# Optimization experiments

Hardware: AMD Instinct MI355X
Metric: run time of the kernel (lower is better)

## Reference

```python
import itertools
import jax, jax.numpy as jnp
import numpy as np

B, S, D = 512, 49, 448
H, KD, RATIO, RES = 8, 32, 4, 7
EKD = KD * RATIO              # expanded key dim = 128
QKV_OUT = H * (2 * KD + EKD)  # 1536
MLP_HID = D * 4               # 1792
EPS = 1e-5
LS_INIT = 1e-5


def _build_bias_idxs():
    points = list(itertools.product(range(RES), range(RES)))
    offsets = {}
    idxs = []
    for p1 in points:
        for p2 in points:
            off = (abs(p1[0] - p2[0]), abs(p1[1] - p2[1]))
            if off not in offsets:
                offsets[off] = len(offsets)
            idxs.append(offsets[off])
    return np.asarray(idxs, dtype=np.int32).reshape(len(points), len(points)), len(offsets)


def setup_inputs() -> dict:
    key = jax.random.key(0)
    ks = jax.random.split(key, 10)
    idxs_np, n_off = _build_bias_idxs()  # (49,49), 49 unique offsets
    std = 0.02
    return {
        "hidden_states": jax.random.normal(ks[0], (B, S, D), jnp.float32),
        "ln1_g": jnp.ones((D,), jnp.float32),
        "ln1_b": jnp.zeros((D,), jnp.float32),
        "qkv_w": jax.random.normal(ks[1], (D, QKV_OUT), jnp.float32) * std,
        "qkv_b": jnp.zeros((QKV_OUT,), jnp.float32),
        "attention_biases": jax.random.normal(ks[2], (H, n_off), jnp.float32) * std,
        "proj_w": jax.random.normal(ks[3], (H * EKD, D), jnp.float32) * std,
        "proj_b": jnp.zeros((D,), jnp.float32),
        "ln2_g": jnp.ones((D,), jnp.float32),
        "ln2_b": jnp.zeros((D,), jnp.float32),
        "mlp_w1": jax.random.normal(ks[4], (D, MLP_HID), jnp.float32) * std,
        "mlp_b1": jnp.zeros((MLP_HID,), jnp.float32),
        "mlp_w2": jax.random.normal(ks[5], (MLP_HID, D), jnp.float32) * std,
        "mlp_b2": jnp.zeros((D,), jnp.float32),
        "ls1": jnp.full((D,), LS_INIT, jnp.float32),
        "ls2": jnp.full((D,), LS_INIT, jnp.float32),
        "attention_bias_idxs": jnp.asarray(idxs_np),
    }


def _layernorm(x, g, b):
    mu = jnp.mean(x, axis=-1, keepdims=True)
    var = jnp.mean(jnp.square(x - mu), axis=-1, keepdims=True)
    return (x - mu) * jax.lax.rsqrt(var + EPS) * g + b


def reference(hidden_states, ln1_g, ln1_b, qkv_w, qkv_b, attention_biases,
              proj_w, proj_b, ln2_g, ln2_b, mlp_w1, mlp_b1, mlp_w2, mlp_b2,
              ls1, ls2, attention_bias_idxs):
    x = hidden_states
    # --- token mixer (self-attention with relative-position bias) ---
    h = _layernorm(x, ln1_g, ln1_b)
    qkv = h @ qkv_w + qkv_b                           # [B,S,1536]
    qkv = qkv.reshape(B, S, H, 2 * KD + EKD)
    q, k, v = jnp.split(qkv, [KD, 2 * KD], axis=3)    # [B,S,H,32/32/128]
    scale = KD ** (-0.5)
    scores = jnp.einsum("bqhd,bkhd->bhqk", q, k) * scale
    bias = attention_biases[:, attention_bias_idxs]   # [H,S,S]
    probs = jax.nn.softmax(scores + bias[None], axis=-1)
    ctx = jnp.einsum("bhqk,bkhd->bqhd", probs, v).reshape(B, S, H * EKD)
    attn_out = ctx @ proj_w + proj_b                  # [B,S,D]
    # --- residual with layerscale (drop_path = identity in eval) ---
    x = x + ls1 * attn_out
    # --- MLP branch ---
    h2 = _layernorm(x, ln2_g, ln2_b)
    m = jax.nn.gelu(h2 @ mlp_w1 + mlp_b1, approximate=False)
    m = m @ mlp_w2 + mlp_b2
    x = x + ls2 * m
    return x
```

## Files before the change

kernel.cpp:

```cpp
#include <hip/hip_runtime.h>
#include <hip/hip_bf16.h>

#define BB 512
#define SS 49
#define DD 448
#define HH 8
#define QKVO 1536
#define MLPH 1792
#define MM (BB*SS)

using bf16_t = __hip_bfloat16;
typedef __attribute__((ext_vector_type(8))) short short8;
typedef __attribute__((ext_vector_type(4))) float f32x4;

__device__ __forceinline__ void gload_lds16(const void* g, void* l) {
  __builtin_amdgcn_global_load_lds(
      (const __attribute__((address_space(1))) void*)g,
      (__attribute__((address_space(3))) void*)l,
      16, 0, 0);
}

__global__ void prep_kernel(const float* __restrict__ qkv_w, const float* __restrict__ proj_w,
                            const float* __restrict__ w1, const float* __restrict__ w2,
                            const float* __restrict__ ab, const int* __restrict__ idxs,
                            bf16_t* __restrict__ qkv_wT, bf16_t* __restrict__ proj_wT,
                            bf16_t* __restrict__ w1T, bf16_t* __restrict__ w2T,
                            bf16_t* __restrict__ bias_pad)
{
  int idx = blockIdx.x * 256 + threadIdx.x;
  if (idx < 688128) {
    int n = idx / 448, k = idx % 448;
    qkv_wT[idx] = __float2bfloat16(qkv_w[k*1536 + n]);
  } else if ((idx -= 688128) < 458752) {
    int n = idx / 1024, k = idx % 1024;
    proj_wT[idx] = __float2bfloat16(proj_w[k*448 + n]);
  } else if ((idx -= 458752) < 802816) {
    int n = idx / 448, k = idx % 448;
    w1T[idx] = __float2bfloat16(w1[k*1792 + n]);
  } else if ((idx -= 802816) < 802816) {
    int n = idx / 1792, k = idx % 1792;
    w2T[idx] = __float2bfloat16(w2[k*448 + n]);
  } else if ((idx -= 802816) < 32768) {
    int h = idx >> 12, r = (idx >> 6) & 63, c = idx & 63;
    float v = (r < SS && c < SS) ? ab[h*49 + idxs[r*49 + c]] : -1e30f;
    bias_pad[idx] = __float2bfloat16(v);
  }
}

__global__ __launch_bounds__(256) void ln_kernel(const float* __restrict__ x,
                                                 const float* __restrict__ g,
                                                 const float* __restrict__ b,
                                                 bf16_t* __restrict__ out)
{
  const int w = threadIdx.x >> 6, lane = threadIdx.x & 63;
  const int row = blockIdx.x * 4 + w;
  const float* xr = x + (size_t)row * DD;
  float v[7];
  float s = 0.f;
#pragma unroll
  for (int j = 0; j < 7; ++j) { v[j] = xr[lane + 64*j]; s += v[j]; }
#pragma unroll
  for (int off = 32; off; off >>= 1) s += __shfl_xor(s, off, 64);
  const float mu = s * (1.0f/448.0f);
  float q = 0.f;
#pragma unroll
  for (int j = 0; j < 7; ++j) { float d = v[j] - mu; q += d*d; }
#pragma unroll
  for (int off = 32; off; off >>= 1) q += __shfl_xor(q, off, 64);
  const float rstd = rsqrtf(q * (1.0f/448.0f) + 1e-5f);
  bf16_t* orow = out + (size_t)row * DD;
#pragma unroll
  for (int j = 0; j < 7; ++j) {
    int c = lane + 64*j;
    orow[c] = __float2bfloat16((v[j] - mu) * rstd * g[c] + b[c]);
  }
}

__global__ __launch_bounds__(256) void red1_ln2_kernel(
    const float* __restrict__ x, const bf16_t* __restrict__ p0,
    const bf16_t* __restrict__ p1, const float* __restrict__ pb,
    const float* __restrict__ ls1, const float* __restrict__ g,
    const float* __restrict__ b, float* __restrict__ out, bf16_t* __restrict__ h2)
{
  const int w = threadIdx.x >> 6, lane = threadIdx.x & 63;
  const int row = blockIdx.x * 4 + w;
  const float* xr = x + (size_t)row * DD;
  const bf16_t* p0r = p0 + (size_t)row * DD;
  const bf16_t* p1r = p1 + (size_t)row * DD;
  float* orow = out + (size_t)row * DD;
  float v[7];
  float s = 0.f;
#pragma unroll
  for (int j = 0; j < 7; ++j) {
    const int c = lane + 64*j;
    const float pv = __bfloat162float(p0r[c]) + __bfloat162float(p1r[c]) + pb[c];
    v[j] = xr[c] + ls1[c] * pv;
    orow[c] = v[j];
    s += v[j];
  }
#pragma unroll
  for (int off = 32; off; off >>= 1) s += __shfl_xor(s, off, 64);
  const float mu = s * (1.0f/448.0f);
  float q = 0.f;
#pragma unroll
  for (int j = 0; j < 7; ++j) { float d = v[j] - mu; q += d*d; }
#pragma unroll
  for (int off = 32; off; off >>= 1) q += __shfl_xor(q, off, 64);
  const float rstd = rsqrtf(q * (1.0f/448.0f) + 1e-5f);
  bf16_t* hrow = h2 + (size_t)row * DD;
#pragma unroll
  for (int j = 0; j < 7; ++j) {
    const int c = lane + 64*j;
    hrow[c] = __float2bfloat16((v[j] - mu) * rstd * g[c] + b[c]);
  }
}

__global__ __launch_bounds__(256) void red2_kernel(
    const bf16_t* __restrict__ q0, const bf16_t* __restrict__ q1,
    const float* __restrict__ pb, const float* __restrict__ ls2,
    float* __restrict__ out)
{
  const int w = threadIdx.x >> 6, lane = threadIdx.x & 63;
  const int row = blockIdx.x * 4 + w;
  const bf16_t* q0r = q0 + (size_t)row * DD;
  const bf16_t* q1r = q1 + (size_t)row * DD;
  float* orow = out + (size_t)row * DD;
#pragma unroll
  for (int j = 0; j < 7; ++j) {
    const int c = lane + 64*j;
    const float pv = __bfloat162float(q0r[c]) + __bfloat162float(q1r[c]) + pb[c];
    orow[c] = orow[c] + ls2[c] * pv;
  }
}

enum { EP_BF16 = 0, EP_GELU = 2, EP_PART = 4 };

template<int EPI, int NSPLIT>
__global__ __launch_bounds__(256, 2) void gemmr_bf16(
    const bf16_t* __restrict__ A, const bf16_t* __restrict__ Bt,
    const float* __restrict__ bias, bf16_t* __restrict__ O0,
    bf16_t* __restrict__ O1, int N, int K, int gy)
{
  __shared__ __align__(16) char lds[32768];
  const int t = threadIdx.x;
  const int lane = t & 63;
  const int w = t >> 6;

  const int chunk = gridDim.x >> 3;
  const int swz = (blockIdx.x & 7) * chunk + (blockIdx.x >> 3);
  const int m0 = (swz / (gy * NSPLIT)) * 128;
  const int rr = swz % (gy * NSPLIT);
  const int n0 = (rr / NSPLIT) * 128;
  const int sp = rr % NSPLIT;
  const int ksub = K / NSPLIT;
  const int kbase = sp * ksub;

  const int fr = lane & 15;
  const int fq = lane >> 4;
  const int wm = (w >> 1) * 64;
  const int wn = (w & 1) * 64;

  f32x4 acc[4][4];
#pragma unroll
  for (int i = 0; i < 4; ++i)
#pragma unroll
    for (int j = 0; j < 4; ++j)
      acc[i][j] = f32x4{0.f, 0.f, 0.f, 0.f};

  const int rsub = t >> 3;
  const int g8 = (t & 7) ^ (rsub & 7);
  const int wbase = w * 1024;
  const int nkt = ksub >> 6;

  const bf16_t* gA[4];
  const bf16_t* gB[4];
#pragma unroll
  for (int i = 0; i < 4; ++i) {
    gA[i] = A + (size_t)(m0 + i*32 + rsub) * K + kbase + g8*8;
    int rb = n0 + i*32 + rsub;
    if (rb >= N) rb = N - 1;
    gB[i] = Bt + (size_t)rb * K + kbase + g8*8;
  }

  for (int kt = 0; kt < nkt; ++kt) {
    const int ko = kt << 6;
#pragma unroll
    for (int i = 0; i < 4; ++i) {
      gload_lds16(gA[i] + ko, lds + i*4096 + wbase);
      gload_lds16(gB[i] + ko, lds + 16384 + i*4096 + wbase);
    }
    __syncthreads();
#pragma unroll
    for (int kk = 0; kk < 2; ++kk) {
      short8 af[4], bfr[4];
#pragma unroll
      for (int i = 0; i < 4; ++i) {
        const int ra = wm + i*16 + fr;
        const int ca = (fq + kk*4) ^ (ra & 7);
        af[i] = *(const short8*)(lds + ra*128 + ca*16);
        const int rb2 = wn + i*16 + fr;
        const int cb = (fq + kk*4) ^ (rb2 & 7);
        bfr[i] = *(const short8*)(lds + 16384 + rb2*128 + cb*16);
      }
#pragma unroll
      for (int mi = 0; mi < 4; ++mi)
#pragma unroll
        for (int ni = 0; ni < 4; ++ni)
          acc[mi][ni] = __builtin_amdgcn_mfma_f32_16x16x32_bf16(af[mi], bfr[ni], acc[mi][ni], 0, 0, 0);
    }
    __syncthreads();
  }

  bf16_t* P = (NSPLIT == 2 && sp == 1) ? O1 : O0;
#pragma unroll
  for (int mi = 0; mi < 4; ++mi) {
#pragma unroll
    for (int ni = 0; ni < 4; ++ni) {
      const int col = n0 + wn + ni*16 + fr;
      if (col < N) {
        float bc = 0.f;
        if constexpr (EPI != EP_PART) bc = bias[col];
        const int row0 = m0 + wm + mi*16 + fq*4;
#pragma unroll
        for (int ri = 0; ri < 4; ++ri) {
          const size_t o = (size_t)(row0 + ri) * N + col;
          const float v = acc[mi][ni][ri] + bc;
          if constexpr (EPI == EP_GELU) {
            P[o] = __float2bfloat16(0.5f * v * (1.0f + erff(v * 0.7071067811865475f)));
          } else {
            P[o] = __float2bfloat16(v);
          }
        }
      }
    }
  }
}

__global__ __launch_bounds__(64) void attn_mfma_kernel(const bf16_t* __restrict__ qkv,
                                                       const bf16_t* __restrict__ bias_pad,
                                                       bf16_t* __restrict__ ctx)
{
  __shared__ __align__(16) bf16_t VsF[64*128];
  __shared__ __align__(16) bf16_t PsF[64*72];
  const int b = blockIdx.x >> 3, h = blockIdx.x & 7;
  const int l = threadIdx.x;
  const int fr = l & 15, g = l >> 4;
  const size_t base = ((size_t)b * SS) * QKVO + (size_t)h * 192;

  for (int c = l; c < 1024; c += 64) {
    const int j = c >> 4, ch = c & 15;
    const int jc = j < SS ? j : SS - 1;
    short8 v = *(const short8*)(qkv + base + (size_t)jc * QKVO + 64 + ch*8);
    *(short8*)(&VsF[j*128 + ((ch ^ (j >> 3)) & 15)*8]) = v;
  }

  short8 qf[4], kf[4];
#pragma unroll
  for (int mi = 0; mi < 4; ++mi) {
    int qr = mi*16 + fr; if (qr > SS-1) qr = SS-1;
    qf[mi] = *(const short8*)(qkv + base + (size_t)qr * QKVO + g*8);
    int kr = mi*16 + fr; if (kr > SS-1) kr = SS-1;
    kf[mi] = *(const short8*)(qkv + base + (size_t)kr * QKVO + 32 + g*8);
  }
  f32x4 sc[4][4];
#pragma unroll
  for (int mi = 0; mi < 4; ++mi)
#pragma unroll
    for (int ni = 0; ni < 4; ++ni)
      sc[mi][ni] = f32x4{0.f,0.f,0.f,0.f};
#pragma unroll
  for (int mi = 0; mi < 4; ++mi)
#pragma unroll
    for (int ni = 0; ni < 4; ++ni)
      sc[mi][ni] = __builtin_amdgcn_mfma_f32_16x16x32_bf16(qf[mi], kf[ni], sc[mi][ni], 0, 0, 0);

  const float scale = 0.17677669529663687f;
  const bf16_t* bp = bias_pad + (size_t)h * 4096;
#pragma unroll
  for (int mi = 0; mi < 4; ++mi) {
#pragma unroll
    for (int ri = 0; ri < 4; ++ri) {
      const int r = mi*16 + g*4 + ri;
      float v0 = sc[mi][0][ri]*scale + __bfloat162float(bp[r*64 +      fr]);
      float v1 = sc[mi][1][ri]*scale + __bfloat162float(bp[r*64 + 16 + fr]);
      float v2 = sc[mi][2][ri]*scale + __bfloat162float(bp[r*64 + 32 + fr]);
      float v3 = sc[mi][3][ri]*scale + __bfloat162float(bp[r*64 + 48 + fr]);
      float m = fmaxf(fmaxf(v0, v1), fmaxf(v2, v3));
#pragma unroll
      for (int off = 8; off; off >>= 1) m = fmaxf(m, __shfl_xor(m, off, 64));
      v0 = __expf(v0 - m); v1 = __expf(v1 - m);
      v2 = __expf(v2 - m); v3 = __expf(v3 - m);
      float s = v0 + v1 + v2 + v3;
#pragma unroll
      for (int off = 8; off; off >>= 1) s += __shfl_xor(s, off, 64);
      const float inv = 1.0f / s;
      PsF[r*72 +      fr] = __float2bfloat16(v0 * inv);
      PsF[r*72 + 16 + fr] = __float2bfloat16(v1 * inv);
      PsF[r*72 + 32 + fr] = __float2bfloat16(v2 * inv);
      PsF[r*72 + 48 + fr] = __float2bfloat16(v3 * inv);
    }
  }
  __syncthreads();

  short8 pf[4][2];
#pragma unroll
  for (int mi = 0; mi < 4; ++mi)
#pragma unroll
    for (int ks = 0; ks < 2; ++ks)
      pf[mi][ks] = *(const short8*)(&PsF[(mi*16 + fr)*72 + ks*32 + g*8]);

#pragma unroll
  for (int ni = 0; ni < 8; ++ni) {
    const int e = ni*16 + fr;
    short8 vf[2];
#pragma unroll
    for (int ks = 0; ks < 2; ++ks) {
      const int jb = ks*32 + g*8;
#pragma unroll
      for (int jj = 0; jj < 8; ++jj) {
        const int j = jb + jj;
        const int ch = ((e >> 3) ^ (j >> 3)) & 15;
        vf[ks][jj] = *(const short*)(&VsF[j*128 + ch*8 + (e & 7)]);
      }
    }
    f32x4 acc2[4];
#pragma unroll
    for (int mi = 0; mi < 4; ++mi) acc2[mi] = f32x4{0.f,0.f,0.f,0.f};
#pragma unroll
    for (int ks = 0; ks < 2; ++ks)
#pragma unroll
      for (int mi = 0; mi < 4; ++mi)
        acc2[mi] = __builtin_amdgcn_mfma_f32_16x16x32_bf16(pf[mi][ks], vf[ks], acc2[mi], 0, 0, 0);
#pragma unroll
    for (int mi = 0; mi < 4; ++mi) {
#pragma unroll
      for (int ri = 0; ri < 4; ++ri) {
        const int q = mi*16 + g*4 + ri;
        if (q < SS)
          ctx[((size_t)b * SS + q) * 1024 + h*128 + e] = __float2bfloat16(acc2[mi][ri]);
      }
    }
  }
}

extern "C" void kernel_launch(void* const* d_in, const int* in_sizes, int n_in,
                              void* d_out, int out_size, void* d_ws, size_t ws_size,
                              hipStream_t stream) {
  const float* x      = (const float*)d_in[0];
  const float* ln1_g  = (const float*)d_in[1];
  const float* ln1_b  = (const float*)d_in[2];
  const float* qkv_w  = (const float*)d_in[3];
  const float* qkv_b  = (const float*)d_in[4];
  const float* ab     = (const float*)d_in[5];
  const float* proj_w = (const float*)d_in[6];
  const float* proj_b = (const float*)d_in[7];
  const float* ln2_g  = (const float*)d_in[8];
  const float* ln2_b  = (const float*)d_in[9];
  const float* w1     = (const float*)d_in[10];
  const float* b1     = (const float*)d_in[11];
  const float* w2     = (const float*)d_in[12];
  const float* b2     = (const float*)d_in[13];
  const float* ls1    = (const float*)d_in[14];
  const float* ls2    = (const float*)d_in[15];
  const int*   idxs   = (const int*)d_in[16];
  float* out = (float*)d_out;
  char* ws = (char*)d_ws;

  bf16_t* h_buf    = (bf16_t*)(ws);
  bf16_t* qkv_buf  = (bf16_t*)(ws + 22478848);
  bf16_t* ctx_buf  = (bf16_t*)(ws + 99549184);
  bf16_t* m_buf    = (bf16_t*)(ws + 22478848);
  bf16_t* p0       = (bf16_t*)(ws + 22478848);
  bf16_t* p1       = (bf16_t*)(ws + 44957696);
  bf16_t* q0       = (bf16_t*)(ws);
  bf16_t* q1       = (bf16_t*)(ws + 112394240);
  bf16_t* qkv_wT   = (bf16_t*)(ws + 150929408);
  bf16_t* proj_wT  = (bf16_t*)(ws + 152305664);
  bf16_t* w1T      = (bf16_t*)(ws + 153223168);
  bf16_t* w2T      = (bf16_t*)(ws + 154828800);
  bf16_t* bias_pad = (bf16_t*)(ws + 156434432);

  const int prep_total = 688128 + 458752 + 802816 + 802816 + 32768;
  prep_kernel<<<(prep_total + 255)/256, 256, 0, stream>>>(
      qkv_w, proj_w, w1, w2, ab, idxs, qkv_wT, proj_wT, w1T, w2T, bias_pad);

  ln_kernel<<<MM/4, 256, 0, stream>>>(x, ln1_g, ln1_b, h_buf);

  gemmr_bf16<EP_BF16, 1><<<196*12, 256, 0, stream>>>(
      h_buf, qkv_wT, qkv_b, qkv_buf, nullptr, QKVO, DD, 12);

  attn_mfma_kernel<<<BB*HH, 64, 0, stream>>>(qkv_buf, bias_pad, ctx_buf);

  gemmr_bf16<EP_PART, 2><<<196*4*2, 256, 0, stream>>>(
      ctx_buf, proj_wT, nullptr, p0, p1, DD, 1024, 4);

  red1_ln2_kernel<<<MM/4, 256, 0, stream>>>(
      x, p0, p1, proj_b, ls1, ln2_g, ln2_b, out, h_buf);

  gemmr_bf16<EP_GELU, 1><<<196*14, 256, 0, stream>>>(
      h_buf, w1T, b1, m_buf, nullptr, MLPH, DD, 14);

  gemmr_bf16<EP_PART, 2><<<196*4*2, 256, 0, stream>>>(
      m_buf, w2T, nullptr, q0, q1, DD, MLPH, 4);

  red2_kernel<<<MM/4, 256, 0, stream>>>(q0, q1, b2, ls2, out);
}
```

Baseline: 324.8 us.

## Fuse weight prep with LN1, vectorize residual kernels, use tanh GELU

```diff
diff --git a/kernel.cpp b/kernel.cpp
--- a/kernel.cpp
+++ b/kernel.cpp
@@ -20,40 +20,46 @@
       16, 0, 0);
 }
 
-__global__ void prep_kernel(const float* __restrict__ qkv_w, const float* __restrict__ proj_w,
-                            const float* __restrict__ w1, const float* __restrict__ w2,
-                            const float* __restrict__ ab, const int* __restrict__ idxs,
-                            bf16_t* __restrict__ qkv_wT, bf16_t* __restrict__ proj_wT,
-                            bf16_t* __restrict__ w1T, bf16_t* __restrict__ w2T,
-                            bf16_t* __restrict__ bias_pad)
+__device__ __forceinline__ float fast_gelu(float v) {
+  const float u = 0.7978845608028654f * (v + 0.044715f * v * v * v);
+  const float e = __expf(2.0f * u);
+  return 0.5f * v * (2.0f - 2.0f / (e + 1.0f));
+}
+
+#define PREP_BLOCKS 10880
+__global__ __launch_bounds__(256) void prep_ln1_kernel(
+    const float* __restrict__ qkv_w, const float* __restrict__ proj_w,
+    const float* __restrict__ w1, const float* __restrict__ w2,
+    const float* __restrict__ ab, const int* __restrict__ idxs,
+    bf16_t* __restrict__ qkv_wT, bf16_t* __restrict__ proj_wT,
+    bf16_t* __restrict__ w1T, bf16_t* __restrict__ w2T,
+    bf16_t* __restrict__ bias_pad,
+    const float* __restrict__ x, const float* __restrict__ g,
+    const float* __restrict__ b, bf16_t* __restrict__ h)
 {
-  int idx = blockIdx.x * 256 + threadIdx.x;
-  if (idx < 688128) {
-    int n = idx / 448, k = idx % 448;
-    qkv_wT[idx] = __float2bfloat16(qkv_w[k*1536 + n]);
-  } else if ((idx -= 688128) < 458752) {
-    int n = idx / 1024, k = idx % 1024;
-    proj_wT[idx] = __float2bfloat16(proj_w[k*448 + n]);
-  } else if ((idx -= 458752) < 802816) {
-    int n = idx / 448, k = idx % 448;
-    w1T[idx] = __float2bfloat16(w1[k*1792 + n]);
-  } else if ((idx -= 802816) < 802816) {
-    int n = idx / 1792, k = idx % 1792;
-    w2T[idx] = __float2bfloat16(w2[k*448 + n]);
-  } else if ((idx -= 802816) < 32768) {
-    int h = idx >> 12, r = (idx >> 6) & 63, c = idx & 63;
-    float v = (r < SS && c < SS) ? ab[h*49 + idxs[r*49 + c]] : -1e30f;
-    bias_pad[idx] = __float2bfloat16(v);
-  }
-}
-
-__global__ __launch_bounds__(256) void ln_kernel(const float* __restrict__ x,
-                                                 const float* __restrict__ g,
-                                                 const float* __restrict__ b,
-                                                 bf16_t* __restrict__ out)
-{
+  if (blockIdx.x < PREP_BLOCKS) {
+    int idx = blockIdx.x * 256 + threadIdx.x;
+    if (idx < 688128) {
+      int n = idx / 448, k = idx % 448;
+      qkv_wT[idx] = __float2bfloat16(qkv_w[k*1536 + n]);
+    } else if ((idx -= 688128) < 458752) {
+      int n = idx / 1024, k = idx % 1024;
+      proj_wT[idx] = __float2bfloat16(proj_w[k*448 + n]);
+    } else if ((idx -= 458752) < 802816) {
+      int n = idx / 448, k = idx % 448;
+      w1T[idx] = __float2bfloat16(w1[k*1792 + n]);
+    } else if ((idx -= 802816) < 802816) {
+      int n = idx / 1792, k = idx % 1792;
+      w2T[idx] = __float2bfloat16(w2[k*448 + n]);
+    } else if ((idx -= 802816) < 32768) {
+      int hh = idx >> 12, r = (idx >> 6) & 63, c = idx & 63;
+      float v = (r < SS && c < SS) ? ab[hh*49 + idxs[r*49 + c]] : -1e30f;
+      bias_pad[idx] = __float2bfloat16(v);
+    }
+    return;
+  }
   const int w = threadIdx.x >> 6, lane = threadIdx.x & 63;
-  const int row = blockIdx.x * 4 + w;
+  const int row = (blockIdx.x - PREP_BLOCKS) * 4 + w;
   const float* xr = x + (size_t)row * DD;
   float v[7];
   float s = 0.f;
@@ -68,7 +74,7 @@
 #pragma unroll
   for (int off = 32; off; off >>= 1) q += __shfl_xor(q, off, 64);
   const float rstd = rsqrtf(q * (1.0f/448.0f) + 1e-5f);
-  bf16_t* orow = out + (size_t)row * DD;
+  bf16_t* orow = h + (size_t)row * DD;
 #pragma unroll
   for (int j = 0; j < 7; ++j) {
     int c = lane + 64*j;
@@ -84,34 +90,58 @@
 {
   const int w = threadIdx.x >> 6, lane = threadIdx.x & 63;
   const int row = blockIdx.x * 4 + w;
-  const float* xr = x + (size_t)row * DD;
-  const bf16_t* p0r = p0 + (size_t)row * DD;
-  const bf16_t* p1r = p1 + (size_t)row * DD;
-  float* orow = out + (size_t)row * DD;
-  float v[7];
+  const float2* x2 = (const float2*)(x + (size_t)row * DD);
+  const uint* p02 = (const uint*)(p0 + (size_t)row * DD);
+  const uint* p12 = (const uint*)(p1 + (size_t)row * DD);
+  const float2* pb2 = (const float2*)pb;
+  const float2* ls2v = (const float2*)ls1;
+  float2* o2 = (float2*)(out + (size_t)row * DD);
+  const int np = (lane < 32) ? 4 : 3;
+  float2 v[4];
   float s = 0.f;
 #pragma unroll
-  for (int j = 0; j < 7; ++j) {
-    const int c = lane + 64*j;
-    const float pv = __bfloat162float(p0r[c]) + __bfloat162float(p1r[c]) + pb[c];
-    v[j] = xr[c] + ls1[c] * pv;
-    orow[c] = v[j];
-    s += v[j];
+  for (int j = 0; j < 4; ++j) {
+    if (j < np) {
+      const int p = (j < 3) ? (lane + 64*j) : (192 + lane);
+      const float2 xv = x2[p];
+      const uint a0 = p02[p], a1 = p12[p];
+      const float2 bb = pb2[p];
+      const float2 ll = ls2v[p];
+      float lo = __bfloat162float(*(const bf16_t*)&a0) + __bfloat162float(*(const bf16_t*)&a1) + bb.x;
+      uint h0 = a0 >> 16, h1 = a1 >> 16;
+      float hi = __bfloat162float(*(const bf16_t*)&h0) + __bfloat162float(*(const bf16_t*)&h1) + bb.y;
+      v[j].x = xv.x + ll.x * lo;
+      v[j].y = xv.y + ll.y * hi;
+      o2[p] = v[j];
+      s += v[j].x + v[j].y;
+    }
   }
 #pragma unroll
   for (int off = 32; off; off >>= 1) s += __shfl_xor(s, off, 64);
   const float mu = s * (1.0f/448.0f);
   float q = 0.f;
 #pragma unroll
-  for (int j = 0; j < 7; ++j) { float d = v[j] - mu; q += d*d; }
+  for (int j = 0; j < 4; ++j) {
+    if (j < np) {
+      float d0 = v[j].x - mu, d1 = v[j].y - mu;
+      q += d0*d0 + d1*d1;
+    }
+  }
 #pragma unroll
   for (int off = 32; off; off >>= 1) q += __shfl_xor(q, off, 64);
   const float rstd = rsqrtf(q * (1.0f/448.0f) + 1e-5f);
-  bf16_t* hrow = h2 + (size_t)row * DD;
-#pragma unroll
-  for (int j = 0; j < 7; ++j) {
-    const int c = lane + 64*j;
-    hrow[c] = __float2bfloat16((v[j] - mu) * rstd * g[c] + b[c]);
+  const float2* g2 = (const float2*)g;
+  const float2* b2v = (const float2*)b;
+  ushort2* h22 = (ushort2*)(h2 + (size_t)row * DD);
+#pragma unroll
+  for (int j = 0; j < 4; ++j) {
+    if (j < np) {
+      const int p = (j < 3) ? (lane + 64*j) : (192 + lane);
+      const float2 gg = g2[p], bbv = b2v[p];
+      bf16_t r0 = __float2bfloat16((v[j].x - mu) * rstd * gg.x + bbv.x);
+      bf16_t r1 = __float2bfloat16((v[j].y - mu) * rstd * gg.y + bbv.y);
+      h22[p] = make_ushort2(*(ushort*)&r0, *(ushort*)&r1);
+    }
   }
 }
 
@@ -122,14 +152,27 @@
 {
   const int w = threadIdx.x >> 6, lane = threadIdx.x & 63;
   const int row = blockIdx.x * 4 + w;
-  const bf16_t* q0r = q0 + (size_t)row * DD;
-  const bf16_t* q1r = q1 + (size_t)row * DD;
-  float* orow = out + (size_t)row * DD;
-#pragma unroll
-  for (int j = 0; j < 7; ++j) {
-    const int c = lane + 64*j;
-    const float pv = __bfloat162float(q0r[c]) + __bfloat162float(q1r[c]) + pb[c];
-    orow[c] = orow[c] + ls2[c] * pv;
+  const uint* q02 = (const uint*)(q0 + (size_t)row * DD);
+  const uint* q12 = (const uint*)(q1 + (size_t)row * DD);
+  const float2* pb2 = (const float2*)pb;
+  const float2* ls2v = (const float2*)ls2;
+  float2* o2 = (float2*)(out + (size_t)row * DD);
+  const int np = (lane < 32) ? 4 : 3;
+#pragma unroll
+  for (int j = 0; j < 4; ++j) {
+    if (j < np) {
+      const int p = (j < 3) ? (lane + 64*j) : (192 + lane);
+      const uint a0 = q02[p], a1 = q12[p];
+      const float2 bb = pb2[p];
+      const float2 ll = ls2v[p];
+      float lo = __bfloat162float(*(const bf16_t*)&a0) + __bfloat162float(*(const bf16_t*)&a1) + bb.x;
+      uint h0 = a0 >> 16, h1 = a1 >> 16;
+      float hi = __bfloat162float(*(const bf16_t*)&h0) + __bfloat162float(*(const bf16_t*)&h1) + bb.y;
+      float2 ov = o2[p];
+      ov.x += ll.x * lo;
+      ov.y += ll.y * hi;
+      o2[p] = ov;
+    }
   }
 }
 
@@ -226,7 +269,7 @@
           const size_t o = (size_t)(row0 + ri) * N + col;
           const float v = acc[mi][ni][ri] + bc;
           if constexpr (EPI == EP_GELU) {
-            P[o] = __float2bfloat16(0.5f * v * (1.0f + erff(v * 0.7071067811865475f)));
+            P[o] = __float2bfloat16(fast_gelu(v));
           } else {
             P[o] = __float2bfloat16(v);
           }
@@ -380,11 +423,9 @@
   bf16_t* w2T      = (bf16_t*)(ws + 154828800);
   bf16_t* bias_pad = (bf16_t*)(ws + 156434432);
 
-  const int prep_total = 688128 + 458752 + 802816 + 802816 + 32768;
-  prep_kernel<<<(prep_total + 255)/256, 256, 0, stream>>>(
-      qkv_w, proj_w, w1, w2, ab, idxs, qkv_wT, proj_wT, w1T, w2T, bias_pad);
-
-  ln_kernel<<<MM/4, 256, 0, stream>>>(x, ln1_g, ln1_b, h_buf);
+  prep_ln1_kernel<<<PREP_BLOCKS + MM/4, 256, 0, stream>>>(
+      qkv_w, proj_w, w1, w2, ab, idxs, qkv_wT, proj_wT, w1T, w2T, bias_pad,
+      x, ln1_g, ln1_b, h_buf);
 
   gemmr_bf16<EP_BF16, 1><<<196*12, 256, 0, stream>>>(
       h_buf, qkv_wT, qkv_b, qkv_buf, nullptr, QKVO, DD, 12);
```

Result: slower. 332.8 us (+2.5%).
